# Kernel optimization log

Measured on AMD Instinct MI355X. Metric: run time of the kernel, lower is better.

Reference implementation:

```python
import jax, jax.numpy as jnp
import numpy as np

EPS = 1e-8

def setup_inputs() -> dict:
    key = jax.random.key(0)
    k0, k1, k2, k3, k4 = jax.random.split(key, 5)
    B, N, K, Q, L, F = 8, 5, 5, 4, 128, 768
    support_emb = jax.random.normal(k0, (B, N, K, L, F), dtype=jnp.float32)
    query_emb = jax.random.normal(k1, (B, N * Q, L, F), dtype=jnp.float32)
    B_mask = jax.random.randint(k2, (B, N, K, L), 0, 2, dtype=jnp.int32)
    I_mask = jax.random.randint(k3, (B, N, K, L), 0, 2, dtype=jnp.int32)
    trigger_label = jax.random.randint(k4, (B, N * Q, L), 0, 2 * N + 1, dtype=jnp.int32)
    return {"support_emb": support_emb, "query_emb": query_emb, "B_mask": B_mask,
            "I_mask": I_mask, "trigger_label": trigger_label, "N": N, "K": K, "Q": Q}

def _proto(support_emb, Bm, Im, N):
    # support_emb: (B,N,K,L,F); Bm/Im: (B,N,K,L) float
    sum_B = jnp.einsum('bnklf,bnkl->bnf', support_emb, Bm)
    cnt_B = Bm.sum((2, 3))[..., None] + EPS
    pB = sum_B / cnt_B                                   # (B,N,F)
    sum_I = jnp.einsum('bnklf,bnkl->bnf', support_emb, Im)
    cnt_I = Im.sum((2, 3))[..., None] + EPS
    pI = sum_I / cnt_I                                   # (B,N,F)
    Om = 1.0 - Bm - Im                                   # (B,N,K,L)
    sum_O = jnp.einsum('bnklf,bnkl->bf', support_emb, Om)
    cnt_O = Om.sum((1, 2, 3))[:, None] + EPS
    pO = sum_O / cnt_O                                   # (B,F)
    Bsz, F = pO.shape
    # interleave: tags [O, B_0, I_0, B_1, I_1, ...]
    pBI = jnp.stack([pB, pI], axis=2).reshape(Bsz, 2 * N, F)
    return jnp.concatenate([pO[:, None, :], pBI], axis=1)  # (B, 2N+1, F)

def reference(support_emb, query_emb, B_mask, I_mask, trigger_label, N, K, Q):
    dt = support_emb.dtype
    Bm = B_mask.astype(dt)
    Im = I_mask.astype(dt)
    prototype = _proto(support_emb, Bm, Im, N)             # (B, 2N+1, F)
    # similarity: broadcast dot product -> batched GEMM
    logits = jnp.einsum('bqlf,btf->bqlt', query_emb, prototype)  # (B, NQ, L, 2N+1)
    T = logits.shape[-1]
    flat = logits.reshape(-1, T)
    pred = jnp.argmax(flat, axis=1)
    lab = trigger_label.reshape(-1)
    logp = jax.nn.log_softmax(flat, axis=-1)
    loss = -jnp.take_along_axis(logp, lab[:, None], axis=1).mean()
    return (loss, logits, pred)
```

## Files before the change

kernel.cpp:

```cpp
#include <hip/hip_runtime.h>
#include <cstdint>
#include <cstddef>

#define EPS 1e-8f

#define Bsz 8
#define Nn  5
#define Kk  5
#define Qq  4
#define Ll  128
#define Ff  768
#define NQ  (Nn*Qq)
#define Tt  (2*Nn+1)
#define KL  (Kk*Ll)
#define ROWS_PER_B (NQ*Ll)
#define NROWS (Bsz*ROWS_PER_B)
#define F4  (Ff/4)

__global__ __launch_bounds__(256) void stage1_partials(
    const float* __restrict__ sup,
    const int*   __restrict__ Bm,
    const int*   __restrict__ Im,
    float* __restrict__ part,
    float* __restrict__ cntB,
    float* __restrict__ cntI,
    int CH, int CHUNK)
{
    int blk  = blockIdx.x;
    int bn   = blk / CH;
    int ch   = blk - bn * CH;
    int pos0 = ch * CHUNK;
    int tid  = threadIdx.x;

    const float* sp = sup + ((size_t)bn * KL + pos0) * Ff;
    const int*   bp = Bm + bn * KL + pos0;
    const int*   ip = Im + bn * KL + pos0;

    __shared__ float smB[KL];
    __shared__ float smI[KL];
    for (int p = tid; p < CHUNK; p += 256) {
        smB[p] = (float)bp[p];
        smI[p] = (float)ip[p];
    }
    __syncthreads();

    float aB0=0,aB1=0,aB2=0, aI0=0,aI1=0,aI2=0, aO0=0,aO1=0,aO2=0;
    const float* r = sp + tid;
    for (int p = 0; p < CHUNK; ++p, r += Ff) {
        float mb = smB[p], mi = smI[p];
        float mo = 1.0f - mb - mi;
        float v0 = r[0], v1 = r[256], v2 = r[512];
        aB0 = fmaf(mb, v0, aB0); aB1 = fmaf(mb, v1, aB1); aB2 = fmaf(mb, v2, aB2);
        aI0 = fmaf(mi, v0, aI0); aI1 = fmaf(mi, v1, aI1); aI2 = fmaf(mi, v2, aI2);
        aO0 = fmaf(mo, v0, aO0); aO1 = fmaf(mo, v1, aO1); aO2 = fmaf(mo, v2, aO2);
    }
    float* o = part + (size_t)blk * (3 * Ff);
    o[tid]          = aB0; o[tid + 256]          = aB1; o[tid + 512]          = aB2;
    o[Ff + tid]     = aI0; o[Ff + tid + 256]     = aI1; o[Ff + tid + 512]     = aI2;
    o[2*Ff + tid]   = aO0; o[2*Ff + tid + 256]   = aO1; o[2*Ff + tid + 512]   = aO2;

    if (tid == 0) { float c = 0; for (int p = 0; p < CHUNK; ++p) c += smB[p]; cntB[blk] = c; }
    if (tid == 1) { float c = 0; for (int p = 0; p < CHUNK; ++p) c += smI[p]; cntI[blk] = c; }
}

__global__ void stage2_proto(
    const float* __restrict__ part,
    const float* __restrict__ cntB,
    const float* __restrict__ cntI,
    float* __restrict__ proto,
    int CH)
{
    int b = blockIdx.x;
    int f = threadIdx.x;

    float sumO = 0.0f, cntO = 0.0f;
    for (int n = 0; n < Nn; ++n) {
        int bn = b * Nn + n;
        float sB = 0, sI = 0, sO = 0, cB = 0, cI = 0;
        for (int ch = 0; ch < CH; ++ch) {
            const float* p = part + (size_t)(bn * CH + ch) * (3 * Ff);
            sB += p[f];
            sI += p[Ff + f];
            sO += p[2 * Ff + f];
            cB += cntB[bn * CH + ch];
            cI += cntI[bn * CH + ch];
        }
        proto[((size_t)b * Tt + (1 + 2 * n)) * Ff + f] = sB / (cB + EPS);
        proto[((size_t)b * Tt + (2 + 2 * n)) * Ff + f] = sI / (cI + EPS);
        sumO += sO;
        cntO += (float)KL - cB - cI;
    }
    proto[(size_t)b * Tt * Ff + f] = sumO / (cntO + EPS);
}

#define BLOCKS_PER_B 80
#define ROWS_PER_WAVE 8

__global__ __launch_bounds__(256) void stage3_logits(
    const float* __restrict__ query,
    const float* __restrict__ proto,
    const int*   __restrict__ label,
    float* __restrict__ out_logits,
    float* __restrict__ out_pred,
    float* __restrict__ loss_out)
{
    __shared__ float4 sp[Tt * F4];
    __shared__ float sLoss;

    int b  = blockIdx.x / BLOCKS_PER_B;
    int rg = blockIdx.x - b * BLOCKS_PER_B;

    if (threadIdx.x == 0) sLoss = 0.0f;
    const float4* pg = (const float4*)(proto + (size_t)b * Tt * Ff);
    for (int i = threadIdx.x; i < Tt * F4; i += 256) sp[i] = pg[i];
    __syncthreads();

    int wave = threadIdx.x >> 6;
    int lane = threadIdx.x & 63;
    int row0 = rg * (4 * ROWS_PER_WAVE) + wave * ROWS_PER_WAVE;

    float wloss = 0.0f;

    for (int r = 0; r < ROWS_PER_WAVE; ++r) {
        int row = row0 + r;
        size_t grow = (size_t)b * ROWS_PER_B + row;
        const float4* q = (const float4*)(query + grow * Ff);
        float4 q0 = q[lane], q1 = q[64 + lane], q2 = q[128 + lane];
        int lab = label[grow];

        float m = -INFINITY, s = 0.0f, labv = 0.0f, bestv = -INFINITY;
        int bestt = 0;
        float myLogit = 0.0f;

        for (int t = 0; t < Tt; ++t) {
            const float4* pv = &sp[t * F4];
            float4 p0 = pv[lane], p1 = pv[64 + lane], p2 = pv[128 + lane];
            float d = q0.x*p0.x + q0.y*p0.y + q0.z*p0.z + q0.w*p0.w
                    + q1.x*p1.x + q1.y*p1.y + q1.z*p1.z + q1.w*p1.w
                    + q2.x*p2.x + q2.y*p2.y + q2.z*p2.z + q2.w*p2.w;
            #pragma unroll
            for (int off = 32; off > 0; off >>= 1) d += __shfl_xor(d, off, 64);
            if (t == lane) myLogit = d;
            if (d > bestv) { bestv = d; bestt = t; }
            float mnew = fmaxf(m, d);
            s = s * __expf(m - mnew) + __expf(d - mnew);
            m = mnew;
            if (t == lab) labv = d;
        }

        if (lane < Tt) out_logits[grow * Tt + lane] = myLogit;
        if (lane == 0) out_pred[grow] = (float)bestt;
        wloss += (m + __logf(s)) - labv;
    }

    if (lane == 0) atomicAdd(&sLoss, wloss);
    __syncthreads();
    if (threadIdx.x == 0) atomicAdd(loss_out, sLoss * (1.0f / (float)NROWS));
}

extern "C" void kernel_launch(void* const* d_in, const int* in_sizes, int n_in,
                              void* d_out, int out_size, void* d_ws, size_t ws_size,
                              hipStream_t stream) {
    const float* sup   = (const float*)d_in[0];
    const float* query = (const float*)d_in[1];
    const int*   Bm    = (const int*)d_in[2];
    const int*   Im    = (const int*)d_in[3];
    const int*   lab   = (const int*)d_in[4];

    int chunk_opts[4] = {32, 64, 128, 640};
    int CHUNK = 640;
    size_t protoFloats = (size_t)Bsz * Tt * Ff;
    for (int i = 0; i < 4; ++i) {
        int c = chunk_opts[i];
        int nblk = (Bsz * Nn) * (KL / c);
        size_t protoOff = (((size_t)nblk * 3 * Ff + 2 * (size_t)nblk) + 3) & ~(size_t)3;
        size_t needBytes = (protoOff + protoFloats) * sizeof(float);
        if (needBytes <= ws_size) { CHUNK = c; break; }
    }
    int CH   = KL / CHUNK;
    int nblk = (Bsz * Nn) * CH;

    float* w     = (float*)d_ws;
    float* part  = w;
    float* cntB  = w + (size_t)nblk * 3 * Ff;
    float* cntI  = cntB + nblk;
    size_t protoOff = (((size_t)nblk * 3 * Ff + 2 * (size_t)nblk) + 3) & ~(size_t)3;
    float* proto = w + protoOff;

    float* loss_out   = (float*)d_out;
    float* out_logits = (float*)d_out + 1;
    float* out_pred   = (float*)d_out + 1 + (size_t)NROWS * Tt;

    hipMemsetAsync(d_out, 0, sizeof(float), stream);

    stage1_partials<<<nblk, 256, 0, stream>>>(sup, Bm, Im, part, cntB, cntI, CH, CHUNK);
    stage2_proto<<<Bsz, Ff, 0, stream>>>(part, cntB, cntI, proto, CH);
    stage3_logits<<<Bsz * BLOCKS_PER_B, 256, 0, stream>>>(query, proto, lab,
                                                          out_logits, out_pred, loss_out);
}
```

Measured before the change: 237.2 us.

## Atomically accumulate prototype partials and hold prototypes in registers for logits

Stage 1 now always uses 32-row chunks and accumulates the partial sums and counts with atomic adds into a per-(b,n) buffer that is zeroed beforehand. Stage 2 therefore only divides instead of reducing over chunks. Stage 3 keeps all prototypes in registers rather than shared memory, computes the 11 dot products together with batched shuffle reductions, and launches twice as many blocks with fewer rows each. The intent is to remove the partial-buffer traffic and the serial per-t reductions, at the cost of atomic contention, higher register pressure, and non-deterministic summation order.

```diff
diff --git a/kernel.cpp b/kernel.cpp
--- a/kernel.cpp
+++ b/kernel.cpp
@@ -16,37 +16,40 @@
 #define ROWS_PER_B (NQ*Ll)
 #define NROWS (Bsz*ROWS_PER_B)
 #define F4  (Ff/4)
+#define BN  (Bsz*Nn)
+
+#define S1_CHUNK 32
+#define S1_CH    (KL / S1_CHUNK)
 
 __global__ __launch_bounds__(256) void stage1_partials(
     const float* __restrict__ sup,
     const int*   __restrict__ Bm,
     const int*   __restrict__ Im,
-    float* __restrict__ part,
-    float* __restrict__ cntB,
-    float* __restrict__ cntI,
-    int CH, int CHUNK)
+    float* __restrict__ accum,
+    float* __restrict__ cnt)
 {
     int blk  = blockIdx.x;
-    int bn   = blk / CH;
-    int ch   = blk - bn * CH;
-    int pos0 = ch * CHUNK;
+    int bn   = blk / S1_CH;
+    int ch   = blk - bn * S1_CH;
+    int pos0 = ch * S1_CHUNK;
     int tid  = threadIdx.x;
 
     const float* sp = sup + ((size_t)bn * KL + pos0) * Ff;
     const int*   bp = Bm + bn * KL + pos0;
     const int*   ip = Im + bn * KL + pos0;
 
-    __shared__ float smB[KL];
-    __shared__ float smI[KL];
-    for (int p = tid; p < CHUNK; p += 256) {
-        smB[p] = (float)bp[p];
-        smI[p] = (float)ip[p];
+    __shared__ float smB[S1_CHUNK];
+    __shared__ float smI[S1_CHUNK];
+    if (tid < S1_CHUNK) {
+        smB[tid] = (float)bp[tid];
+        smI[tid] = (float)ip[tid];
     }
     __syncthreads();
 
     float aB0=0,aB1=0,aB2=0, aI0=0,aI1=0,aI2=0, aO0=0,aO1=0,aO2=0;
     const float* r = sp + tid;
-    for (int p = 0; p < CHUNK; ++p, r += Ff) {
+    #pragma unroll 4
+    for (int p = 0; p < S1_CHUNK; ++p, r += Ff) {
         float mb = smB[p], mi = smI[p];
         float mo = 1.0f - mb - mi;
         float v0 = r[0], v1 = r[256], v2 = r[512];
@@ -54,47 +57,39 @@
         aI0 = fmaf(mi, v0, aI0); aI1 = fmaf(mi, v1, aI1); aI2 = fmaf(mi, v2, aI2);
         aO0 = fmaf(mo, v0, aO0); aO1 = fmaf(mo, v1, aO1); aO2 = fmaf(mo, v2, aO2);
     }
-    float* o = part + (size_t)blk * (3 * Ff);
-    o[tid]          = aB0; o[tid + 256]          = aB1; o[tid + 512]          = aB2;
-    o[Ff + tid]     = aI0; o[Ff + tid + 256]     = aI1; o[Ff + tid + 512]     = aI2;
-    o[2*Ff + tid]   = aO0; o[2*Ff + tid + 256]   = aO1; o[2*Ff + tid + 512]   = aO2;
+    float* o = accum + (size_t)bn * (3 * Ff);
+    atomicAdd(&o[tid],            aB0); atomicAdd(&o[tid + 256],          aB1); atomicAdd(&o[tid + 512],          aB2);
+    atomicAdd(&o[Ff + tid],       aI0); atomicAdd(&o[Ff + tid + 256],     aI1); atomicAdd(&o[Ff + tid + 512],     aI2);
+    atomicAdd(&o[2*Ff + tid],     aO0); atomicAdd(&o[2*Ff + tid + 256],   aO1); atomicAdd(&o[2*Ff + tid + 512],   aO2);
 
-    if (tid == 0) { float c = 0; for (int p = 0; p < CHUNK; ++p) c += smB[p]; cntB[blk] = c; }
-    if (tid == 1) { float c = 0; for (int p = 0; p < CHUNK; ++p) c += smI[p]; cntI[blk] = c; }
+    if (tid == 0) { float c = 0; for (int p = 0; p < S1_CHUNK; ++p) c += smB[p]; atomicAdd(&cnt[bn*2],   c); }
+    if (tid == 1) { float c = 0; for (int p = 0; p < S1_CHUNK; ++p) c += smI[p]; atomicAdd(&cnt[bn*2+1], c); }
 }
 
 __global__ void stage2_proto(
-    const float* __restrict__ part,
-    const float* __restrict__ cntB,
-    const float* __restrict__ cntI,
-    float* __restrict__ proto,
-    int CH)
+    const float* __restrict__ accum,
+    const float* __restrict__ cnt,
+    float* __restrict__ proto)
 {
     int b = blockIdx.x;
     int f = threadIdx.x;
 
     float sumO = 0.0f, cntO = 0.0f;
+    #pragma unroll
     for (int n = 0; n < Nn; ++n) {
         int bn = b * Nn + n;
-        float sB = 0, sI = 0, sO = 0, cB = 0, cI = 0;
-        for (int ch = 0; ch < CH; ++ch) {
-            const float* p = part + (size_t)(bn * CH + ch) * (3 * Ff);
-            sB += p[f];
-            sI += p[Ff + f];
-            sO += p[2 * Ff + f];
-            cB += cntB[bn * CH + ch];
-            cI += cntI[bn * CH + ch];
-        }
-        proto[((size_t)b * Tt + (1 + 2 * n)) * Ff + f] = sB / (cB + EPS);
-        proto[((size_t)b * Tt + (2 + 2 * n)) * Ff + f] = sI / (cI + EPS);
-        sumO += sO;
+        const float* a = accum + (size_t)bn * (3 * Ff);
+        float cB = cnt[bn*2], cI = cnt[bn*2+1];
+        proto[((size_t)b * Tt + (1 + 2 * n)) * Ff + f] = a[f]        / (cB + EPS);
+        proto[((size_t)b * Tt + (2 + 2 * n)) * Ff + f] = a[Ff + f]   / (cI + EPS);
+        sumO += a[2*Ff + f];
         cntO += (float)KL - cB - cI;
     }
     proto[(size_t)b * Tt * Ff + f] = sumO / (cntO + EPS);
 }
 
-#define BLOCKS_PER_B 80
-#define ROWS_PER_WAVE 8
+#define S3_BLOCKS_PER_B 160
+#define S3_ROWS_PER_WAVE 4
 
 __global__ __launch_bounds__(256) void stage3_logits(
     const float* __restrict__ query,
@@ -104,52 +99,66 @@
     float* __restrict__ out_pred,
     float* __restrict__ loss_out)
 {
-    __shared__ float4 sp[Tt * F4];
     __shared__ float sLoss;
 
-    int b  = blockIdx.x / BLOCKS_PER_B;
-    int rg = blockIdx.x - b * BLOCKS_PER_B;
+    int b  = blockIdx.x / S3_BLOCKS_PER_B;
+    int rg = blockIdx.x - b * S3_BLOCKS_PER_B;
+    int wave = threadIdx.x >> 6;
+    int lane = threadIdx.x & 63;
 
     if (threadIdx.x == 0) sLoss = 0.0f;
-    const float4* pg = (const float4*)(proto + (size_t)b * Tt * Ff);
-    for (int i = threadIdx.x; i < Tt * F4; i += 256) sp[i] = pg[i];
     __syncthreads();
 
-    int wave = threadIdx.x >> 6;
-    int lane = threadIdx.x & 63;
-    int row0 = rg * (4 * ROWS_PER_WAVE) + wave * ROWS_PER_WAVE;
+    const float4* pg = (const float4*)(proto + (size_t)b * Tt * Ff);
+    float4 P[Tt][3];
+    #pragma unroll
+    for (int t = 0; t < Tt; ++t) {
+        P[t][0] = pg[t * F4 + lane];
+        P[t][1] = pg[t * F4 + 64 + lane];
+        P[t][2] = pg[t * F4 + 128 + lane];
+    }
 
+    int row0 = rg * (4 * S3_ROWS_PER_WAVE) + wave * S3_ROWS_PER_WAVE;
     float wloss = 0.0f;
 
-    for (int r = 0; r < ROWS_PER_WAVE; ++r) {
-        int row = row0 + r;
-        size_t grow = (size_t)b * ROWS_PER_B + row;
+    for (int r = 0; r < S3_ROWS_PER_WAVE; ++r) {
+        size_t grow = (size_t)b * ROWS_PER_B + row0 + r;
         const float4* q = (const float4*)(query + grow * Ff);
         float4 q0 = q[lane], q1 = q[64 + lane], q2 = q[128 + lane];
         int lab = label[grow];
 
-        float m = -INFINITY, s = 0.0f, labv = 0.0f, bestv = -INFINITY;
-        int bestt = 0;
-        float myLogit = 0.0f;
+        float acc[Tt];
+        #pragma unroll
+        for (int t = 0; t < Tt; ++t) {
+            float d;
+            d = q0.x * P[t][0].x;
+            d = fmaf(q0.y, P[t][0].y, d); d = fmaf(q0.z, P[t][0].z, d); d = fmaf(q0.w, P[t][0].w, d);
+            d = fmaf(q1.x, P[t][1].x, d); d = fmaf(q1.y, P[t][1].y, d);
+            d = fmaf(q1.z, P[t][1].z, d); d = fmaf(q1.w, P[t][1].w, d);
+            d = fmaf(q2.x, P[t][2].x, d); d = fmaf(q2.y, P[t][2].y, d);
+            d = fmaf(q2.z, P[t][2].z, d); d = fmaf(q2.w, P[t][2].w, d);
+            acc[t] = d;
+        }
+        #pragma unroll
+        for (int off = 32; off > 0; off >>= 1) {
+            #pragma unroll
+            for (int t = 0; t < Tt; ++t) acc[t] += __shfl_xor(acc[t], off, 64);
+        }
+        float m = acc[0]; int bt = 0;
+        #pragma unroll
+        for (int t = 1; t < Tt; ++t) if (acc[t] > m) { m = acc[t]; bt = t; }
+        float s = 0.0f;
+        #pragma unroll
+        for (int t = 0; t < Tt; ++t) s += __expf(acc[t] - m);
+        float labv = acc[0];
+        #pragma unroll
+        for (int t = 1; t < Tt; ++t) labv = (lab == t) ? acc[t] : labv;
+        float myv = acc[0];
+        #pragma unroll
+        for (int t = 1; t < Tt; ++t) myv = (lane == t) ? acc[t] : myv;
 
-        for (int t = 0; t < Tt; ++t) {
-            const float4* pv = &sp[t * F4];
-            float4 p0 = pv[lane], p1 = pv[64 + lane], p2 = pv[128 + lane];
-            float d = q0.x*p0.x + q0.y*p0.y + q0.z*p0.z + q0.w*p0.w
-                    + q1.x*p1.x + q1.y*p1.y + q1.z*p1.z + q1.w*p1.w
-                    + q2.x*p2.x + q2.y*p2.y + q2.z*p2.z + q2.w*p2.w;
-            #pragma unroll
-            for (int off = 32; off > 0; off >>= 1) d += __shfl_xor(d, off, 64);
-            if (t == lane) myLogit = d;
-            if (d > bestv) { bestv = d; bestt = t; }
-            float mnew = fmaxf(m, d);
-            s = s * __expf(m - mnew) + __expf(d - mnew);
-            m = mnew;
-            if (t == lab) labv = d;
-        }
-
-        if (lane < Tt) out_logits[grow * Tt + lane] = myLogit;
-        if (lane == 0) out_pred[grow] = (float)bestt;
+        if (lane < Tt) out_logits[grow * Tt + lane] = myv;
+        if (lane == 0) out_pred[grow] = (float)bt;
         wloss += (m + __logf(s)) - labv;
     }
 
@@ -167,34 +176,21 @@
     const int*   Im    = (const int*)d_in[3];
     const int*   lab   = (const int*)d_in[4];
 
-    int chunk_opts[4] = {32, 64, 128, 640};
-    int CHUNK = 640;
-    size_t protoFloats = (size_t)Bsz * Tt * Ff;
-    for (int i = 0; i < 4; ++i) {
-        int c = chunk_opts[i];
-        int nblk = (Bsz * Nn) * (KL / c);
-        size_t protoOff = (((size_t)nblk * 3 * Ff + 2 * (size_t)nblk) + 3) & ~(size_t)3;
-        size_t needBytes = (protoOff + protoFloats) * sizeof(float);
-        if (needBytes <= ws_size) { CHUNK = c; break; }
-    }
-    int CH   = KL / CHUNK;
-    int nblk = (Bsz * Nn) * CH;
-
     float* w     = (float*)d_ws;
-    float* part  = w;
-    float* cntB  = w + (size_t)nblk * 3 * Ff;
-    float* cntI  = cntB + nblk;
-    size_t protoOff = (((size_t)nblk * 3 * Ff + 2 * (size_t)nblk) + 3) & ~(size_t)3;
-    float* proto = w + protoOff;
+    float* accum = w;
+    float* cnt   = accum + (size_t)BN * 3 * Ff;
+    float* proto = cnt + 2 * BN;
+    size_t zeroBytes = ((size_t)BN * 3 * Ff + 2 * BN) * sizeof(float);
 
     float* loss_out   = (float*)d_out;
     float* out_logits = (float*)d_out + 1;
     float* out_pred   = (float*)d_out + 1 + (size_t)NROWS * Tt;
 
+    hipMemsetAsync(d_ws, 0, zeroBytes, stream);
     hipMemsetAsync(d_out, 0, sizeof(float), stream);
 
-    stage1_partials<<<nblk, 256, 0, stream>>>(sup, Bm, Im, part, cntB, cntI, CH, CHUNK);
-    stage2_proto<<<Bsz, Ff, 0, stream>>>(part, cntB, cntI, proto, CH);
-    stage3_logits<<<Bsz * BLOCKS_PER_B, 256, 0, stream>>>(query, proto, lab,
-                                                          out_logits, out_pred, loss_out);
+    stage1_partials<<<BN * S1_CH, 256, 0, stream>>>(sup, Bm, Im, accum, cnt);
+    stage2_proto<<<Bsz, Ff, 0, stream>>>(accum, cnt, proto);
+    stage3_logits<<<Bsz * S3_BLOCKS_PER_B, 256, 0, stream>>>(query, proto, lab,
+                                                             out_logits, out_pred, loss_out);
 }
```

Measured after the change: 208.8 us. 12.0% less time.
